# Kernel optimization log

Hardware: AMD Instinct MI355X
Metric: run time of the kernel (lower is better)

## Reference

```python
import jax, jax.numpy as jnp
import numpy as np

B, S, H, D, HID = 1024, 64, 32, 32, 1024
COMP = 256          # smolgen compress_size
TOK = 32            # smolgen token_compress out dim
LN_EPS = 1e-5


def _xavier(key, shape):
    fan_in, fan_out = shape[0], shape[-1]
    std = np.sqrt(2.0 / (fan_in + fan_out))
    return jax.random.normal(key, shape, dtype=jnp.float32) * std


def setup_inputs() -> dict:
    key = jax.random.key(0)
    ks = jax.random.split(key, 12)
    x = jax.random.normal(ks[0], (B, S, HID), dtype=jnp.float32)
    # attention projections (stored [in, out], no bias on qkv)
    Wq = _xavier(ks[1], (HID, H * D))
    Wk = _xavier(ks[2], (HID, H * D))
    Wv = _xavier(ks[3], (HID, H * D))
    Wo = _xavier(ks[4], (H * D, HID))
    bo = jnp.zeros((HID,), dtype=jnp.float32)
    pos_bias = jnp.zeros((H, S, S), dtype=jnp.float32)
    # smolgen params
    tc_W = _xavier(ks[5], (HID, TOK))                  # token_compress, no bias
    pc_W = _xavier(ks[6], (S * TOK, COMP))             # position_compress linear
    pc_b = jnp.zeros((COMP,), dtype=jnp.float32)
    ln_g = jnp.ones((COMP,), dtype=jnp.float32)        # LayerNorm gamma
    ln_b = jnp.zeros((COMP,), dtype=jnp.float32)       # LayerNorm beta
    hp_W = jax.vmap(lambda k: _xavier(k, (COMP, COMP)))(jax.random.split(ks[7], H))  # [H,COMP,COMP]
    hp_b = jnp.zeros((H, COMP), dtype=jnp.float32)
    alp_W = _xavier(ks[8], (COMP, S * S))              # attention_logits_proj
    alp_b = jnp.zeros((S * S,), dtype=jnp.float32)
    return dict(x=x, Wq=Wq, Wk=Wk, Wv=Wv, Wo=Wo, bo=bo, pos_bias=pos_bias,
                tc_W=tc_W, pc_W=pc_W, pc_b=pc_b, ln_g=ln_g, ln_b=ln_b,
                hp_W=hp_W, hp_b=hp_b, alp_W=alp_W, alp_b=alp_b)


def _smolgen(x, tc_W, pc_W, pc_b, ln_g, ln_b, hp_W, hp_b, alp_W, alp_b):
    b = x.shape[0]
    flat = (x @ tc_W).reshape(b, S * TOK)              # [B, 64*32]
    pv = jax.nn.relu(flat @ pc_W + pc_b)               # [B, COMP]
    mu = jnp.mean(pv, axis=-1, keepdims=True)
    var = jnp.mean(jnp.square(pv - mu), axis=-1, keepdims=True)
    pv = (pv - mu) * jax.lax.rsqrt(var + LN_EPS) * ln_g + ln_b
    # per-head projections, vectorized over heads
    hv = jnp.einsum('bc,hcd->bhd', pv, hp_W) + hp_b    # [B, H, COMP]
    logits = jnp.einsum('bhd,de->bhe', hv, alp_W) + alp_b
    return logits.reshape(b, H, S, S)


def reference(x, Wq, Wk, Wv, Wo, bo, pos_bias, tc_W, pc_W, pc_b, ln_g, ln_b,
              hp_W, hp_b, alp_W, alp_b):
    b = x.shape[0]
    scale = 1.0 / np.sqrt(D)
    q = (x @ Wq).reshape(b, S, H, D).transpose(0, 2, 1, 3)  # [B,H,S,D]
    k = (x @ Wk).reshape(b, S, H, D).transpose(0, 2, 1, 3)
    v = (x @ Wv).reshape(b, S, H, D).transpose(0, 2, 1, 3)
    scores = jnp.einsum('bhqd,bhkd->bhqk', q, k) * scale
    scores = scores + pos_bias[None]
    scores = scores + _smolgen(x, tc_W, pc_W, pc_b, ln_g, ln_b, hp_W, hp_b, alp_W, alp_b)
    attn = jax.nn.softmax(scores, axis=-1)
    out = jnp.einsum('bhqk,bhkd->bhqd', attn, v)             # [B,H,S,D]
    out = out.transpose(0, 2, 1, 3).reshape(b, S, H * D)
    return out @ Wo + bo
```

## Files before the change

kernel.cpp:

```cpp
#include <hip/hip_runtime.h>
#include <hip/hip_bf16.h>
#include <cstdint>
#include <cstddef>

typedef __attribute__((ext_vector_type(4))) float f32x4;
typedef __attribute__((ext_vector_type(8))) short short8;
typedef unsigned short u16;
typedef __attribute__((ext_vector_type(8))) unsigned short u16x8;
typedef __attribute__((ext_vector_type(4))) unsigned short u16x4;

__device__ __forceinline__ u16 f2bf(float f) {
  union { float f; unsigned u; } v; v.f = f;
  unsigned r = v.u + 0x7FFFu + ((v.u >> 16) & 1u);
  return (u16)(r >> 16);
}
__device__ __forceinline__ float bf2f(u16 h) {
  union { unsigned u; float f; } v; v.u = ((unsigned)h) << 16;
  return v.f;
}
__device__ __forceinline__ void gload16(const u16* g, const u16* l) {
  __builtin_amdgcn_global_load_lds((const __attribute__((address_space(1))) void*)g,
                                   (__attribute__((address_space(3))) void*)l, 16, 0, 0);
}
__device__ __forceinline__ void fenced_barrier() {
  __builtin_amdgcn_sched_barrier(0);
  __builtin_amdgcn_s_barrier();
  __builtin_amdgcn_sched_barrier(0);
}

__global__ __launch_bounds__(256) void prep_w2t(
    const float* __restrict__ Wq, const float* __restrict__ Wk, const float* __restrict__ Wv,
    const float* __restrict__ tc, u16* __restrict__ W2t)
{
  __shared__ float t[32][33];
  const int tx = threadIdx.x, ty = threadIdx.y;
  const int k0 = blockIdx.x * 32, n0 = blockIdx.y * 32;
  const float* src = nullptr; int col = 0, sw = 0;
  if      (n0 < 1024) { src = Wq; col = n0;        sw = 1024; }
  else if (n0 < 2048) { src = Wk; col = n0 - 1024; sw = 1024; }
  else if (n0 < 3072) { src = Wv; col = n0 - 2048; sw = 1024; }
  else if (n0 < 3104) { src = tc; col = n0 - 3072; sw = 32;   }
  if (src) {
    #pragma unroll
    for (int r = 0; r < 4; r++) {
      int k = k0 + ty + r * 8;
      t[ty + r * 8][tx] = src[(size_t)k * sw + col + tx];
    }
  }
  __syncthreads();
  #pragma unroll
  for (int r = 0; r < 4; r++) {
    int n = n0 + ty + r * 8, k = k0 + tx;
    u16 v = src ? f2bf(t[tx][ty + r * 8]) : (u16)0;
    W2t[(size_t)n * 1024 + k] = v;
  }
}

__global__ __launch_bounds__(256) void transpose_bf(
    const float* __restrict__ src, u16* __restrict__ dst, int R, int C)
{
  __shared__ float t[32][33];
  const int tx = threadIdx.x, ty = threadIdx.y;
  const size_t zoff = (size_t)blockIdx.z * R * C;
  src += zoff; dst += zoff;
  const int c0 = blockIdx.x * 32, r0 = blockIdx.y * 32;
  #pragma unroll
  for (int r = 0; r < 4; r++)
    t[ty + r * 8][tx] = src[(size_t)(r0 + ty + r * 8) * C + c0 + tx];
  __syncthreads();
  #pragma unroll
  for (int r = 0; r < 4; r++)
    dst[(size_t)(c0 + ty + r * 8) * R + r0 + tx] = f2bf(t[tx][ty + r * 8]);
}

__global__ __launch_bounds__(256) void cvt_x(const float* __restrict__ x, u16* __restrict__ A2)
{
  size_t i = (size_t)blockIdx.x * 256 + threadIdx.x;
  f32x4 v = ((const f32x4*)x)[i];
  u16x4 o;
  #pragma unroll
  for (int j = 0; j < 4; j++) o[j] = f2bf(v[j]);
  ((u16x4*)A2)[i] = o;
}

template<int MODE, int K>
__global__ __launch_bounds__(512, 4) void gemm_p(
    const u16* __restrict__ A, const u16* __restrict__ Bt,
    void* __restrict__ o0, void* __restrict__ o1, void* __restrict__ o2, void* __restrict__ o3,
    const float* __restrict__ bias0, const float* __restrict__ bias1)
{
  __shared__ __align__(16) u16 lds[3][12288];
  const int tid = threadIdx.x;
  const int wid = tid >> 6, lane = tid & 63;
  const int wm = wid >> 1, wn = wid & 1;
  const int g = lane >> 4, l15 = lane & 15;

  const int GX = gridDim.x;
  const int nwg = GX * (int)gridDim.y;
  const int lin = (int)blockIdx.y * GX + (int)blockIdx.x;
  const int swz = (lin & 7) * (nwg >> 3) + (lin >> 3);
  const int bn = swz % GX, bm = swz / GX;

  const int lR = lane >> 3;
  const int logi = (lane & 7) ^ lR;
  const int shb = logi >> 2;
  const int sg = logi & 3;

  const u16* pA0 = A + (size_t)(bm * 256 + shb * 128 + (wid * 2 + 0) * 8 + lR) * K + sg * 8;
  const u16* pA1 = A + (size_t)(bm * 256 + shb * 128 + (wid * 2 + 1) * 8 + lR) * K + sg * 8;
  const u16* pB  = Bt + (size_t)(bn * 128 + shb * 64 + wid * 8 + lR) * K + sg * 8;

  const int aRd = ((wm & 1) * 64 + l15) * 64 + ((((wm >> 1) << 2) | g) ^ (l15 & 7)) * 8;
  const int bRd = 8192 + l15 * 64 + ((((wn << 2) | g) ^ (l15 & 7)) * 8);

  f32x4 acc[4][4];
  #pragma unroll
  for (int i = 0; i < 4; i++)
    #pragma unroll
    for (int j = 0; j < 4; j++)
      #pragma unroll
      for (int r = 0; r < 4; r++) acc[i][j][r] = 0.f;

  constexpr int NT = K >> 5;
  static_assert((NT - 2) % 3 == 0, "unroll-3 requires NT-2 divisible by 3");

#define STG(buf, kt) do {                                                   \
    gload16(pA0 + (size_t)(kt) * 32, &lds[buf][(wid * 2 + 0) * 512]);       \
    gload16(pA1 + (size_t)(kt) * 32, &lds[buf][(wid * 2 + 1) * 512]);       \
    gload16(pB  + (size_t)(kt) * 32, &lds[buf][8192 + wid * 512]); } while (0)

#define ITER(T_, RB_, WB_, DO_STG, VM) do {                                 \
    asm volatile("s_waitcnt vmcnt(" #VM ")" ::: "memory");                  \
    fenced_barrier();                                                       \
    short8 af[4], bfr[4];                                                   \
    _Pragma("unroll")                                                       \
    for (int f_ = 0; f_ < 4; f_++)                                          \
      af[f_] = *(const short8*)&lds[RB_][aRd + f_ * 1024];                  \
    _Pragma("unroll")                                                       \
    for (int n_ = 0; n_ < 4; n_++)                                          \
      bfr[n_] = *(const short8*)&lds[RB_][bRd + n_ * 1024];                 \
    if (DO_STG) STG(WB_, (T_) + 2);                                         \
    asm volatile("s_waitcnt lgkmcnt(0)" ::: "memory");                      \
    __builtin_amdgcn_sched_barrier(0);                                      \
    __builtin_amdgcn_s_setprio(1);                                          \
    _Pragma("unroll")                                                       \
    for (int f_ = 0; f_ < 4; f_++)                                          \
      _Pragma("unroll")                                                     \
      for (int n_ = 0; n_ < 4; n_++)                                        \
        acc[f_][n_] = __builtin_amdgcn_mfma_f32_16x16x32_bf16(              \
            af[f_], bfr[n_], acc[f_][n_], 0, 0, 0);                         \
    __builtin_amdgcn_s_setprio(0);                                          \
  } while (0)

  STG(0, 0); STG(1, 1);

  for (int tb = 0; tb < NT - 2; tb += 3) {
    ITER(tb + 0, 0, 2, true, 3);
    ITER(tb + 1, 1, 0, true, 3);
    ITER(tb + 2, 2, 1, true, 3);
  }
  ITER(NT - 2, 0, 0, false, 3);
  ITER(NT - 1, 1, 0, false, 0);
#undef ITER
#undef STG

  const int lr = lane >> 4, lc = lane & 15;
  #pragma unroll
  for (int fm = 0; fm < 4; fm++) {
    #pragma unroll
    for (int fn = 0; fn < 4; fn++) {
      #pragma unroll
      for (int r = 0; r < 4; r++) {
        int gm = bm * 256 + wm * 64 + fm * 16 + lr * 4 + r;
        int gn = bn * 128 + wn * 64 + fn * 16 + lc;
        float val = acc[fm][fn][r];
        if (MODE == 0) {
          int b = gm >> 6, s = gm & 63;
          if (gn < 3072) {
            int which = gn >> 10, hh = (gn >> 5) & 31, d = gn & 31;
            u16* dst = (which == 0) ? (u16*)o0 : (which == 1) ? (u16*)o1 : (u16*)o2;
            dst[(((size_t)b * 32 + hh) * 64 + s) * 32 + d] = f2bf(val);
          } else if (gn < 3104) {
            ((u16*)o3)[(size_t)b * 2048 + s * 32 + (gn - 3072)] = f2bf(val);
          }
        } else if (MODE == 3) {
          ((u16*)o0)[(size_t)gm * 4096 + gn] = f2bf(val + bias0[gn] + bias1[(gm & 31) * 4096 + gn]);
        } else {
          ((float*)o0)[(size_t)gm * 1024 + gn] = val + bias0[gn];
        }
      }
    }
  }
}

template<int MODE>
__global__ __launch_bounds__(256) void gemm_bt(
    const u16* __restrict__ A, const u16* __restrict__ Bt, int K,
    void* __restrict__ o0, const float* __restrict__ bias0)
{
  __shared__ __align__(16) u16 lA[128 * 32];
  __shared__ __align__(16) u16 lB[128 * 32];
  const int tid = threadIdx.x;
  const int wid = tid >> 6, lane = tid & 63;
  const int wm = wid >> 1, wn = wid & 1;
  const int bn = blockIdx.x, bm = blockIdx.y;
  if (MODE == 2) Bt += (size_t)blockIdx.z * 256 * 256;

  f32x4 acc[4][4];
  #pragma unroll
  for (int i = 0; i < 4; i++)
    #pragma unroll
    for (int j = 0; j < 4; j++)
      #pragma unroll
      for (int r = 0; r < 4; r++) acc[i][j][r] = 0.f;

  const u16* Arow = A + (size_t)(bm * 128) * K;
  const u16* Brow = Bt + (size_t)(bn * 128) * K;

  for (int k0 = 0; k0 < K; k0 += 32) {
    #pragma unroll
    for (int i = 0; i < 2; i++) {
      int c = wid * 128 + i * 64 + lane;
      int row = c >> 2, col = (c & 3) * 8;
      gload16(Arow + (size_t)row * K + k0 + col, &lA[(wid * 128 + i * 64) * 8]);
      gload16(Brow + (size_t)row * K + k0 + col, &lB[(wid * 128 + i * 64) * 8]);
    }
    __syncthreads();
    short8 af[4], bfr[4];
    #pragma unroll
    for (int f = 0; f < 4; f++) {
      af[f]  = *(const short8*)&lA[(wm * 64 + f * 16 + (lane & 15)) * 32 + (lane >> 4) * 8];
      bfr[f] = *(const short8*)&lB[(wn * 64 + f * 16 + (lane & 15)) * 32 + (lane >> 4) * 8];
    }
    #pragma unroll
    for (int fm = 0; fm < 4; fm++)
      #pragma unroll
      for (int fn = 0; fn < 4; fn++)
        acc[fm][fn] = __builtin_amdgcn_mfma_f32_16x16x32_bf16(af[fm], bfr[fn], acc[fm][fn], 0, 0, 0);
    __syncthreads();
  }

  const int lr = lane >> 4, lc = lane & 15;
  #pragma unroll
  for (int fm = 0; fm < 4; fm++) {
    #pragma unroll
    for (int fn = 0; fn < 4; fn++) {
      #pragma unroll
      for (int r = 0; r < 4; r++) {
        int gm = bm * 128 + wm * 64 + fm * 16 + lr * 4 + r;
        int gn = bn * 128 + wn * 64 + fn * 16 + lc;
        float val = acc[fm][fn][r];
        if (MODE == 1) {
          float v = val + bias0[gn];
          ((float*)o0)[(size_t)gm * 256 + gn] = v > 0.f ? v : 0.f;
        } else if (MODE == 2) {
          int h = blockIdx.z;
          ((u16*)o0)[((size_t)gm * 32 + h) * 256 + gn] = f2bf(val + bias0[h * 256 + gn]);
        }
      }
    }
  }
}

__global__ __launch_bounds__(256) void ln_kernel(
    const float* __restrict__ pv, const float* __restrict__ g, const float* __restrict__ b2,
    u16* __restrict__ out)
{
  __shared__ float red[256];
  const int bi = blockIdx.x, t = threadIdx.x;
  float v = pv[(size_t)bi * 256 + t];
  red[t] = v; __syncthreads();
  #pragma unroll
  for (int o = 128; o > 0; o >>= 1) { if (t < o) red[t] += red[t + o]; __syncthreads(); }
  float mu = red[0] * (1.f / 256.f);
  __syncthreads();
  float dv = v - mu;
  red[t] = dv * dv; __syncthreads();
  #pragma unroll
  for (int o = 128; o > 0; o >>= 1) { if (t < o) red[t] += red[t + o]; __syncthreads(); }
  float var = red[0] * (1.f / 256.f);
  float rs = rsqrtf(var + 1e-5f);
  out[(size_t)bi * 256 + t] = f2bf(dv * rs * g[t] + b2[t]);
}

__global__ __launch_bounds__(64) void attn_mfma(
    const u16* __restrict__ qb, const u16* __restrict__ kb, const u16* __restrict__ vb,
    const u16* __restrict__ lg, u16* __restrict__ aout)
{
  __shared__ __align__(16) u16 vT[32 * 64];
  __shared__ __align__(16) u16 Pl[64 * 64];
  const int bid = blockIdx.x;
  const int lane = threadIdx.x;
  const int g = lane >> 4, l15 = lane & 15;
  const size_t base = (size_t)bid * 2048;

  {
    const u16* vrow = vb + base + lane * 32;
    u16x8 vv[4];
    #pragma unroll
    for (int c = 0; c < 4; c++) vv[c] = *(const u16x8*)(vrow + c * 8);
    #pragma unroll
    for (int d = 0; d < 32; d++)
      vT[d * 64 + (lane ^ ((d & 7) << 3))] = vv[d >> 3][d & 7];
  }

  short8 qf[4], kf[4];
  #pragma unroll
  for (int t = 0; t < 4; t++) {
    qf[t] = *(const short8*)(qb + base + (size_t)(t * 16 + l15) * 32 + g * 8);
    kf[t] = *(const short8*)(kb + base + (size_t)(t * 16 + l15) * 32 + g * 8);
  }

  f32x4 s[4][4];
  #pragma unroll
  for (int tm = 0; tm < 4; tm++)
    #pragma unroll
    for (int tn = 0; tn < 4; tn++)
      #pragma unroll
      for (int r = 0; r < 4; r++) s[tm][tn][r] = 0.f;
  #pragma unroll
  for (int tm = 0; tm < 4; tm++)
    #pragma unroll
    for (int tn = 0; tn < 4; tn++)
      s[tm][tn] = __builtin_amdgcn_mfma_f32_16x16x32_bf16(kf[tm], qf[tn], s[tm][tn], 0, 0, 0);

  const float scale = 0.17677669529663687f;
  float inv4[4];
  const u16* lbase = lg + (size_t)bid * 4096;
  #pragma unroll
  for (int tn = 0; tn < 4; tn++) {
    const int q = tn * 16 + l15;
    float mx = -1e30f;
    #pragma unroll
    for (int tm = 0; tm < 4; tm++) {
      u16x4 u = *(const u16x4*)(lbase + (size_t)q * 64 + tm * 16 + g * 4);
      #pragma unroll
      for (int r = 0; r < 4; r++) {
        s[tm][tn][r] = s[tm][tn][r] * scale + bf2f(u[r]);
        mx = fmaxf(mx, s[tm][tn][r]);
      }
    }
    mx = fmaxf(mx, __shfl_xor(mx, 16));
    mx = fmaxf(mx, __shfl_xor(mx, 32));
    float sm = 0.f;
    #pragma unroll
    for (int tm = 0; tm < 4; tm++)
      #pragma unroll
      for (int r = 0; r < 4; r++) {
        float e = __expf(s[tm][tn][r] - mx);
        s[tm][tn][r] = e;
        sm += e;
      }
    sm += __shfl_xor(sm, 16);
    sm += __shfl_xor(sm, 32);
    inv4[tn] = 1.f / sm;
    #pragma unroll
    for (int tm = 0; tm < 4; tm++) {
      u16x4 p;
      #pragma unroll
      for (int r = 0; r < 4; r++) p[r] = f2bf(s[tm][tn][r]);
      *(u16x4*)&Pl[q * 64 + ((tm * 16 + g * 4) ^ ((q & 7) << 3))] = p;
    }
  }
  __syncthreads();

  f32x4 o[2][4];
  #pragma unroll
  for (int md = 0; md < 2; md++)
    #pragma unroll
    for (int tn = 0; tn < 4; tn++)
      #pragma unroll
      for (int r = 0; r < 4; r++) o[md][tn][r] = 0.f;
  #pragma unroll
  for (int ks = 0; ks < 2; ks++) {
    short8 vf2[2], pf[4];
    #pragma unroll
    for (int md = 0; md < 2; md++)
      vf2[md] = *(const short8*)&vT[(md * 16 + l15) * 64 + ((ks * 32 + g * 8) ^ ((l15 & 7) << 3))];
    #pragma unroll
    for (int tn = 0; tn < 4; tn++)
      pf[tn] = *(const short8*)&Pl[(tn * 16 + l15) * 64 + ((ks * 32 + g * 8) ^ ((l15 & 7) << 3))];
    #pragma unroll
    for (int md = 0; md < 2; md++)
      #pragma unroll
      for (int tn = 0; tn < 4; tn++)
        o[md][tn] = __builtin_amdgcn_mfma_f32_16x16x32_bf16(vf2[md], pf[tn], o[md][tn], 0, 0, 0);
  }

  const int b = bid >> 5, h = bid & 31;
  #pragma unroll
  for (int md = 0; md < 2; md++) {
    #pragma unroll
    for (int tn = 0; tn < 4; tn++) {
      const int q = tn * 16 + l15, d0 = md * 16 + g * 4;
      u16x4 u;
      #pragma unroll
      for (int r = 0; r < 4; r++) u[r] = f2bf(o[md][tn][r] * inv4[tn]);
      *(u16x4*)(aout + ((size_t)(b * 64 + q)) * 1024 + h * 32 + d0) = u;
    }
  }
}

extern "C" void kernel_launch(void* const* d_in, const int* in_sizes, int n_in,
                              void* d_out, int out_size, void* d_ws, size_t ws_size,
                              hipStream_t stream) {
  const float* x       = (const float*)d_in[0];
  const float* Wq      = (const float*)d_in[1];
  const float* Wk      = (const float*)d_in[2];
  const float* Wv      = (const float*)d_in[3];
  const float* Wo      = (const float*)d_in[4];
  const float* bo      = (const float*)d_in[5];
  const float* pos_b   = (const float*)d_in[6];
  const float* tc_W    = (const float*)d_in[7];
  const float* pc_W    = (const float*)d_in[8];
  const float* pc_b    = (const float*)d_in[9];
  const float* ln_g    = (const float*)d_in[10];
  const float* ln_b    = (const float*)d_in[11];
  const float* hp_W    = (const float*)d_in[12];
  const float* hp_b    = (const float*)d_in[13];
  const float* alp_W   = (const float*)d_in[14];
  const float* alp_b   = (const float*)d_in[15];
  float* out = (float*)d_out;

  char* w = (char*)d_ws;
  u16* A2     = (u16*)w;
  u16* logits = (u16*)w;              w += 268435456;
  u16* qb     = (u16*)w;              w += 134217728;
  u16* kb     = (u16*)w;              w += 134217728;
  u16* vb     = (u16*)w;              w += 134217728;
  u16* aout   = (u16*)w;              w += 134217728;
  u16* W2t    = (u16*)w;              w += (size_t)3200 * 1024 * 2;
  u16* pcWt   = (u16*)w;              w += (size_t)256 * 2048 * 2;
  u16* hpWt   = (u16*)w;              w += (size_t)32 * 256 * 256 * 2;
  u16* alpWt  = (u16*)w;              w += (size_t)4096 * 256 * 2;
  u16* WoT    = (u16*)w;              w += (size_t)1024 * 1024 * 2;
  u16* flatb  = (u16*)w;              w += (size_t)1024 * 2048 * 2;
  float* pvtmp= (float*)w;            w += (size_t)1024 * 256 * 4;
  u16* pvb    = (u16*)w;              w += (size_t)1024 * 256 * 2;
  u16* hvb    = (u16*)w;              w += (size_t)32768 * 256 * 2;

  prep_w2t    <<<dim3(32, 100),    dim3(32, 8), 0, stream>>>(Wq, Wk, Wv, tc_W, W2t);
  transpose_bf<<<dim3(8, 64, 1),   dim3(32, 8), 0, stream>>>(pc_W, pcWt, 2048, 256);
  transpose_bf<<<dim3(8, 8, 32),   dim3(32, 8), 0, stream>>>(hp_W, hpWt, 256, 256);
  transpose_bf<<<dim3(128, 8, 1),  dim3(32, 8), 0, stream>>>(alp_W, alpWt, 256, 4096);
  transpose_bf<<<dim3(32, 32, 1),  dim3(32, 8), 0, stream>>>(Wo, WoT, 1024, 1024);
  cvt_x       <<<65536, 256, 0, stream>>>(x, A2);

  gemm_p<0, 1024> <<<dim3(25, 256),  512, 0, stream>>>(A2, W2t, qb, kb, vb, flatb, nullptr, nullptr);
  gemm_bt<1>      <<<dim3(2, 8),     256, 0, stream>>>(flatb, pcWt, 2048, pvtmp, pc_b);
  ln_kernel       <<<1024, 256, 0, stream>>>(pvtmp, ln_g, ln_b, pvb);
  gemm_bt<2>      <<<dim3(2, 8, 32), 256, 0, stream>>>(pvb, hpWt, 256, hvb, hp_b);
  gemm_p<3, 256>  <<<dim3(32, 128),  512, 0, stream>>>(hvb, alpWt, logits, nullptr, nullptr, nullptr, alp_b, pos_b);
  attn_mfma       <<<32768, 64, 0, stream>>>(qb, kb, vb, logits, aout);
  gemm_p<4, 1024> <<<dim3(8, 256),   512, 0, stream>>>(aout, WoT, out, nullptr, nullptr, nullptr, bo, nullptr);
}
```

Before: 1.086 ms.

## Merge prep kernels into one launch and split-K the position_compress GEMM

Folds the x conversion and all weight transposes into a single prep_all launch, indexed by block id, to cut five kernel launches. The position_compress GEMM, which had only 16 blocks, is split eight ways along K so it launches 128 blocks. Each split writes its own fp32 partial buffer, and ln_kernel sums the partials and applies bias and ReLU before the layer norm. This costs extra workspace and partial-buffer traffic in exchange for better GPU occupancy on a small GEMM.

```diff
diff --git a/kernel.cpp b/kernel.cpp
--- a/kernel.cpp
+++ b/kernel.cpp
@@ -28,42 +28,61 @@
   __builtin_amdgcn_sched_barrier(0);
 }
 
-__global__ __launch_bounds__(256) void prep_w2t(
+__global__ __launch_bounds__(256) void prep_all(
     const float* __restrict__ Wq, const float* __restrict__ Wk, const float* __restrict__ Wv,
-    const float* __restrict__ tc, u16* __restrict__ W2t)
+    const float* __restrict__ tc, const float* __restrict__ pc_W, const float* __restrict__ hp_W,
+    const float* __restrict__ alp_W, const float* __restrict__ Wo, const float* __restrict__ x,
+    u16* __restrict__ W2t, u16* __restrict__ pcWt, u16* __restrict__ hpWt,
+    u16* __restrict__ alpWt, u16* __restrict__ WoT, u16* __restrict__ A2)
 {
   __shared__ float t[32][33];
-  const int tx = threadIdx.x, ty = threadIdx.y;
-  const int k0 = blockIdx.x * 32, n0 = blockIdx.y * 32;
-  const float* src = nullptr; int col = 0, sw = 0;
-  if      (n0 < 1024) { src = Wq; col = n0;        sw = 1024; }
-  else if (n0 < 2048) { src = Wk; col = n0 - 1024; sw = 1024; }
-  else if (n0 < 3072) { src = Wv; col = n0 - 2048; sw = 1024; }
-  else if (n0 < 3104) { src = tc; col = n0 - 3072; sw = 32;   }
-  if (src) {
+  const int tid = threadIdx.x;
+  int bid = blockIdx.x;
+
+  if (bid < 65536) {
+    size_t i = (size_t)bid * 256 + tid;
+    f32x4 v = ((const f32x4*)x)[i];
+    u16x4 o;
+    #pragma unroll
+    for (int j = 0; j < 4; j++) o[j] = f2bf(v[j]);
+    ((u16x4*)A2)[i] = o;
+    return;
+  }
+  bid -= 65536;
+  const int tx = tid & 31, ty = tid >> 5;
+
+  if (bid < 3200) {
+    const int k0 = (bid & 31) * 32, n0 = (bid >> 5) * 32;
+    const float* src = nullptr; int col = 0, sw = 0;
+    if      (n0 < 1024) { src = Wq; col = n0;        sw = 1024; }
+    else if (n0 < 2048) { src = Wk; col = n0 - 1024; sw = 1024; }
+    else if (n0 < 3072) { src = Wv; col = n0 - 2048; sw = 1024; }
+    else if (n0 < 3104) { src = tc; col = n0 - 3072; sw = 32;   }
+    if (src) {
+      #pragma unroll
+      for (int r = 0; r < 4; r++)
+        t[ty + r * 8][tx] = src[(size_t)(k0 + ty + r * 8) * sw + col + tx];
+    }
+    __syncthreads();
     #pragma unroll
     for (int r = 0; r < 4; r++) {
-      int k = k0 + ty + r * 8;
-      t[ty + r * 8][tx] = src[(size_t)k * sw + col + tx];
-    }
-  }
-  __syncthreads();
-  #pragma unroll
-  for (int r = 0; r < 4; r++) {
-    int n = n0 + ty + r * 8, k = k0 + tx;
-    u16 v = src ? f2bf(t[tx][ty + r * 8]) : (u16)0;
-    W2t[(size_t)n * 1024 + k] = v;
-  }
-}
-
-__global__ __launch_bounds__(256) void transpose_bf(
-    const float* __restrict__ src, u16* __restrict__ dst, int R, int C)
-{
-  __shared__ float t[32][33];
-  const int tx = threadIdx.x, ty = threadIdx.y;
-  const size_t zoff = (size_t)blockIdx.z * R * C;
-  src += zoff; dst += zoff;
-  const int c0 = blockIdx.x * 32, r0 = blockIdx.y * 32;
+      int n = n0 + ty + r * 8, k = k0 + tx;
+      u16 v = src ? f2bf(t[tx][ty + r * 8]) : (u16)0;
+      W2t[(size_t)n * 1024 + k] = v;
+    }
+    return;
+  }
+  bid -= 3200;
+  const float* src; u16* dst; int R, C, gx, gy, zz = 0;
+  if (bid < 512)       { src = pc_W;  dst = pcWt;  R = 2048; C = 256;  gx = bid & 7;   gy = bid >> 3; }
+  else if (bid < 2560) { int i = bid - 512;  src = hp_W;  dst = hpWt;  R = 256;  C = 256;
+                         gx = i & 7; gy = (i >> 3) & 7; zz = i >> 6; }
+  else if (bid < 3584) { int i = bid - 2560; src = alp_W; dst = alpWt; R = 256;  C = 4096;
+                         gx = i & 127; gy = i >> 7; }
+  else                 { int i = bid - 3584; src = Wo;    dst = WoT;   R = 1024; C = 1024;
+                         gx = i & 31; gy = i >> 5; }
+  src += (size_t)zz * R * C; dst += (size_t)zz * R * C;
+  const int c0 = gx * 32, r0 = gy * 32;
   #pragma unroll
   for (int r = 0; r < 4; r++)
     t[ty + r * 8][tx] = src[(size_t)(r0 + ty + r * 8) * C + c0 + tx];
@@ -71,16 +90,6 @@
   #pragma unroll
   for (int r = 0; r < 4; r++)
     dst[(size_t)(c0 + ty + r * 8) * R + r0 + tx] = f2bf(t[tx][ty + r * 8]);
-}
-
-__global__ __launch_bounds__(256) void cvt_x(const float* __restrict__ x, u16* __restrict__ A2)
-{
-  size_t i = (size_t)blockIdx.x * 256 + threadIdx.x;
-  f32x4 v = ((const f32x4*)x)[i];
-  u16x4 o;
-  #pragma unroll
-  for (int j = 0; j < 4; j++) o[j] = f2bf(v[j]);
-  ((u16x4*)A2)[i] = o;
 }
 
 template<int MODE, int K>
@@ -195,7 +204,7 @@
 
 template<int MODE>
 __global__ __launch_bounds__(256) void gemm_bt(
-    const u16* __restrict__ A, const u16* __restrict__ Bt, int K,
+    const u16* __restrict__ A, const u16* __restrict__ Bt, int kstride, int klen,
     void* __restrict__ o0, const float* __restrict__ bias0)
 {
   __shared__ __align__(16) u16 lA[128 * 32];
@@ -203,8 +212,10 @@
   const int tid = threadIdx.x;
   const int wid = tid >> 6, lane = tid & 63;
   const int wm = wid >> 1, wn = wid & 1;
-  const int bn = blockIdx.x, bm = blockIdx.y;
-  if (MODE == 2) Bt += (size_t)blockIdx.z * 256 * 256;
+  const int bn = blockIdx.x, bm = blockIdx.y, z = blockIdx.z;
+  if (MODE == 2) Bt += (size_t)z * 256 * 256;
+  const int kbeg = (MODE == 1) ? z * 256 : 0;
+  float* opart = (MODE == 1) ? ((float*)o0) + (size_t)z * 1024 * 256 : (float*)o0;
 
   f32x4 acc[4][4];
   #pragma unroll
@@ -214,16 +225,16 @@
       #pragma unroll
       for (int r = 0; r < 4; r++) acc[i][j][r] = 0.f;
 
-  const u16* Arow = A + (size_t)(bm * 128) * K;
-  const u16* Brow = Bt + (size_t)(bn * 128) * K;
-
-  for (int k0 = 0; k0 < K; k0 += 32) {
+  const u16* Arow = A + (size_t)(bm * 128) * kstride + kbeg;
+  const u16* Brow = Bt + (size_t)(bn * 128) * kstride + kbeg;
+
+  for (int k0 = 0; k0 < klen; k0 += 32) {
     #pragma unroll
     for (int i = 0; i < 2; i++) {
       int c = wid * 128 + i * 64 + lane;
       int row = c >> 2, col = (c & 3) * 8;
-      gload16(Arow + (size_t)row * K + k0 + col, &lA[(wid * 128 + i * 64) * 8]);
-      gload16(Brow + (size_t)row * K + k0 + col, &lB[(wid * 128 + i * 64) * 8]);
+      gload16(Arow + (size_t)row * kstride + k0 + col, &lA[(wid * 128 + i * 64) * 8]);
+      gload16(Brow + (size_t)row * kstride + k0 + col, &lB[(wid * 128 + i * 64) * 8]);
     }
     __syncthreads();
     short8 af[4], bfr[4];
@@ -251,11 +262,9 @@
         int gn = bn * 128 + wn * 64 + fn * 16 + lc;
         float val = acc[fm][fn][r];
         if (MODE == 1) {
-          float v = val + bias0[gn];
-          ((float*)o0)[(size_t)gm * 256 + gn] = v > 0.f ? v : 0.f;
+          opart[(size_t)gm * 256 + gn] = val;
         } else if (MODE == 2) {
-          int h = blockIdx.z;
-          ((u16*)o0)[((size_t)gm * 32 + h) * 256 + gn] = f2bf(val + bias0[h * 256 + gn]);
+          ((u16*)o0)[((size_t)gm * 32 + z) * 256 + gn] = f2bf(val + bias0[z * 256 + gn]);
         }
       }
     }
@@ -263,12 +272,16 @@
 }
 
 __global__ __launch_bounds__(256) void ln_kernel(
-    const float* __restrict__ pv, const float* __restrict__ g, const float* __restrict__ b2,
-    u16* __restrict__ out)
+    const float* __restrict__ pv8, const float* __restrict__ pcb,
+    const float* __restrict__ g, const float* __restrict__ b2, u16* __restrict__ out)
 {
   __shared__ float red[256];
   const int bi = blockIdx.x, t = threadIdx.x;
-  float v = pv[(size_t)bi * 256 + t];
+  float v = 0.f;
+  #pragma unroll
+  for (int z = 0; z < 8; z++) v += pv8[(size_t)z * 262144 + (size_t)bi * 256 + t];
+  v += pcb[t];
+  v = v > 0.f ? v : 0.f;
   red[t] = v; __syncthreads();
   #pragma unroll
   for (int o = 128; o > 0; o >>= 1) { if (t < o) red[t] += red[t + o]; __syncthreads(); }
@@ -435,21 +448,17 @@
   u16* alpWt  = (u16*)w;              w += (size_t)4096 * 256 * 2;
   u16* WoT    = (u16*)w;              w += (size_t)1024 * 1024 * 2;
   u16* flatb  = (u16*)w;              w += (size_t)1024 * 2048 * 2;
-  float* pvtmp= (float*)w;            w += (size_t)1024 * 256 * 4;
+  float* pv8  = (float*)w;            w += (size_t)8 * 1024 * 256 * 4;
   u16* pvb    = (u16*)w;              w += (size_t)1024 * 256 * 2;
   u16* hvb    = (u16*)w;              w += (size_t)32768 * 256 * 2;
 
-  prep_w2t    <<<dim3(32, 100),    dim3(32, 8), 0, stream>>>(Wq, Wk, Wv, tc_W, W2t);
-  transpose_bf<<<dim3(8, 64, 1),   dim3(32, 8), 0, stream>>>(pc_W, pcWt, 2048, 256);
-  transpose_bf<<<dim3(8, 8, 32),   dim3(32, 8), 0, stream>>>(hp_W, hpWt, 256, 256);
-  transpose_bf<<<dim3(128, 8, 1),  dim3(32, 8), 0, stream>>>(alp_W, alpWt, 256, 4096);
-  transpose_bf<<<dim3(32, 32, 1),  dim3(32, 8), 0, stream>>>(Wo, WoT, 1024, 1024);
-  cvt_x       <<<65536, 256, 0, stream>>>(x, A2);
+  prep_all<<<73344, 256, 0, stream>>>(Wq, Wk, Wv, tc_W, pc_W, hp_W, alp_W, Wo, x,
+                                      W2t, pcWt, hpWt, alpWt, WoT, A2);
 
   gemm_p<0, 1024> <<<dim3(25, 256),  512, 0, stream>>>(A2, W2t, qb, kb, vb, flatb, nullptr, nullptr);
-  gemm_bt<1>      <<<dim3(2, 8),     256, 0, stream>>>(flatb, pcWt, 2048, pvtmp, pc_b);
-  ln_kernel       <<<1024, 256, 0, stream>>>(pvtmp, ln_g, ln_b, pvb);
-  gemm_bt<2>      <<<dim3(2, 8, 32), 256, 0, stream>>>(pvb, hpWt, 256, hvb, hp_b);
+  gemm_bt<1>      <<<dim3(2, 8, 8),  256, 0, stream>>>(flatb, pcWt, 2048, 256, pv8, nullptr);
+  ln_kernel       <<<1024, 256, 0, stream>>>(pv8, pc_b, ln_g, ln_b, pvb);
+  gemm_bt<2>      <<<dim3(2, 8, 32), 256, 0, stream>>>(pvb, hpWt, 256, 256, hvb, hp_b);
   gemm_p<3, 256>  <<<dim3(32, 128),  512, 0, stream>>>(hvb, alpWt, logits, nullptr, nullptr, nullptr, alp_b, pos_b);
   attn_mfma       <<<32768, 64, 0, stream>>>(qb, kb, vb, logits, aout);
   gemm_p<4, 1024> <<<dim3(8, 256),   512, 0, stream>>>(aout, WoT, out, nullptr, nullptr, nullptr, bo, nullptr);
```

Measured after the change: 1.047 ms, median of 2. 3.6% less time.
